# Kernel tuning notes

Hardware: AMD Instinct MI355X
Metric: run time of the kernel (lower is better)

The kernel has to match this reference:

```python
import math
import jax, jax.numpy as jnp
import numpy as np

B, S, HID = 2, 1024, 4096
NH, NKV, HD = 32, 8, 128
G = NH // NKV            # query heads per KV head (GQA group size)
PAST = 1024              # tokens already in the cache per sequence
L = PAST + S             # total KV tokens attended per sequence
SLOTS = 16384            # paged KV-cache slots (flat token addressing)
MAXPOS = 8192
THETA = 10000.0


def _rope_table():
    inv_freq = 1.0 / (THETA ** (np.arange(0, HD, 2, dtype=np.float64) / HD))
    freqs = np.arange(MAXPOS, dtype=np.float64)[:, None] * inv_freq[None, :]
    emb = np.concatenate([freqs, freqs], axis=-1)          # [MAXPOS, HD]
    return jnp.asarray(np.stack([np.cos(emb), np.sin(emb)], axis=1), jnp.float32)  # [MAXPOS,2,HD]


def setup_inputs() -> dict:
    key = jax.random.key(0)
    ks = jax.random.split(key, 6)
    hidden_states = jax.random.normal(ks[0], (B, S, HID), jnp.float32)
    kv_cache = jax.random.normal(ks[1], (SLOTS, 2, NKV, HD), jnp.float32)  # [slot, k/v, kv_head, hd]
    rope_cache = _rope_table()
    Wq = jax.random.normal(ks[2], (HID, NH * HD), jnp.float32) * 0.02
    Wk = jax.random.normal(ks[3], (HID, NKV * HD), jnp.float32) * 0.02
    Wv = jax.random.normal(ks[4], (HID, NKV * HD), jnp.float32) * 0.02
    Wo = jax.random.normal(ks[5], (NH * HD, HID), jnp.float32) * 0.02
    position_offsets = jnp.full((B,), PAST, jnp.int32)
    base = jnp.arange(B, dtype=jnp.int32)[:, None] * L            # each seq owns L contiguous slots
    kv_drain_addr_lut = base + PAST + jnp.arange(S, dtype=jnp.int32)[None, :]  # [B,S] write addrs
    kv_lut = base + jnp.arange(L, dtype=jnp.int32)[None, :]                    # [B,L] read addrs
    return {
        "hidden_states": hidden_states, "kv_cache": kv_cache, "rope_cache": rope_cache,
        "Wq": Wq, "Wk": Wk, "Wv": Wv, "Wo": Wo,
        "position_offsets": position_offsets,
        "kv_drain_addr_lut": kv_drain_addr_lut, "kv_lut": kv_lut,
    }


def _apply_rope(x, cos, sin):
    # x: [B, H, S, HD]; cos/sin: [B, 1, S, HD]
    x1, x2 = x[..., : HD // 2], x[..., HD // 2:]
    return x * cos + jnp.concatenate([-x2, x1], axis=-1) * sin


def reference(hidden_states, kv_cache, rope_cache, Wq, Wk, Wv, Wo,
              position_offsets, kv_drain_addr_lut, kv_lut):
    # QKV projections
    q = (hidden_states @ Wq).reshape(B, S, NH, HD).transpose(0, 2, 1, 3)    # [B,NH,S,HD]
    k = (hidden_states @ Wk).reshape(B, S, NKV, HD).transpose(0, 2, 1, 3)   # [B,NKV,S,HD]
    v = (hidden_states @ Wv).reshape(B, S, NKV, HD).transpose(0, 2, 1, 3)
    # RoPE at absolute positions
    pos = position_offsets[:, None] + jnp.arange(S, dtype=jnp.int32)        # [B,S]
    cos = rope_cache[pos, 0][:, None]                                       # [B,1,S,HD]
    sin = rope_cache[pos, 1][:, None]
    q = _apply_rope(q, cos, sin)
    k = _apply_rope(k, cos, sin)
    # LUT-addressed KV-cache drain (copy_kv_block)
    k_tok = k.transpose(0, 2, 1, 3).reshape(B * S, NKV, HD)
    v_tok = v.transpose(0, 2, 1, 3).reshape(B * S, NKV, HD)
    lut = kv_drain_addr_lut.reshape(-1)
    kv_cache = kv_cache.at[lut, 0].set(k_tok).at[lut, 1].set(v_tok)
    # Gather per-sequence KV pages and run grouped (GQA) causal attention
    kv = kv_cache[kv_lut]                                                   # [B,L,2,NKV,HD]
    keys = kv[:, :, 0].transpose(0, 2, 1, 3)                                # [B,NKV,L,HD]
    vals = kv[:, :, 1].transpose(0, 2, 1, 3)
    qg = q.reshape(B, NKV, G, S, HD)
    scores = jnp.einsum('bhgsd,bhld->bhgsl', qg, keys) * (HD ** -0.5)       # [B,NKV,G,S,L]
    kpos = jnp.arange(L, dtype=jnp.int32)
    causal = kpos[None, None, :] <= pos[:, :, None]                         # [B,S,L]
    scores = jnp.where(causal[:, None, None], scores, jnp.float32(-1e30))
    p = jax.nn.softmax(scores, axis=-1)
    out = jnp.einsum('bhgsl,bhld->bhgsd', p, vals).reshape(B, NH, S, HD)
    out = out.transpose(0, 2, 1, 3).reshape(B, S, HID)
    return out @ Wo
```

## Files before the change

kernel.cpp:

```cpp
#include <hip/hip_runtime.h>
#include <hip/hip_bf16.h>
#include <cstdint>
#include <cstddef>

#define B_    2
#define S_    1024
#define HID_  4096
#define NH_   32
#define NKV_  8
#define HD_   128
#define G_    4
#define PAST_ 1024
#define L_    2048
#define NQKV_ 6144

typedef __bf16 bf16_t;
typedef bf16_t bf16x4 __attribute__((ext_vector_type(4)));
typedef bf16_t bf16x8 __attribute__((ext_vector_type(8)));
typedef float  f32x4  __attribute__((ext_vector_type(4)));

__device__ __forceinline__ void gload_lds16(const bf16_t* g, bf16_t* l) {
  __builtin_amdgcn_global_load_lds(
      (const __attribute__((address_space(1))) void*)g,
      (__attribute__((address_space(3))) void*)l, 16, 0, 0);
}

__global__ __launch_bounds__(256) void cvt_bf16x8(const float* __restrict__ src,
                                                  bf16_t* __restrict__ dst) {
  size_t i = ((size_t)blockIdx.x * 256 + threadIdx.x) * 8;
  f32x4 a = *(const f32x4*)(src + i);
  f32x4 b = *(const f32x4*)(src + i + 4);
  bf16x8 o;
#pragma unroll
  for (int j = 0; j < 4; ++j) o[j] = (bf16_t)a[j];
#pragma unroll
  for (int j = 0; j < 4; ++j) o[4 + j] = (bf16_t)b[j];
  *(bf16x8*)(dst + i) = o;
}

__global__ __launch_bounds__(256) void transpose_cvt(const float* __restrict__ src,
                                                     bf16_t* __restrict__ dst,
                                                     int R, int C) {
  __shared__ float T[64][65];
  const int tid = threadIdx.x;
  const int c0 = blockIdx.x * 64;
  const int r0 = blockIdx.y * 64;
#pragma unroll
  for (int i = 0; i < 16; ++i) {
    int idx = i * 256 + tid;
    int lr = idx >> 6, lc = idx & 63;
    T[lr][lc] = src[(size_t)(r0 + lr) * C + c0 + lc];
  }
  __syncthreads();
#pragma unroll
  for (int i = 0; i < 16; ++i) {
    int idx = i * 256 + tid;
    int lr = idx >> 6, lc = idx & 63;
    dst[(size_t)(c0 + lr) * R + r0 + lc] = (bf16_t)T[lc][lr];
  }
}

template <bool OUT_BF16>
__global__ __launch_bounds__(256) void gemm_bt(const bf16_t* __restrict__ A,
                                               const bf16_t* __restrict__ Bt,
                                               void* __restrict__ C, int N, int K) {
  __shared__ bf16_t As[128 * 32];
  __shared__ bf16_t Bs[128 * 32];
  const int tid = threadIdx.x;
  const int lane = tid & 63;
  const int w = tid >> 6;
  const int wm = w >> 1, wn = w & 1;
  const int m0 = blockIdx.y * 128;
  const int n0 = blockIdx.x * 128;
  const int g = lane >> 4;
  const int r16 = lane & 15;

  f32x4 acc[4][4] = {};

  for (int kt = 0; kt < K; kt += 32) {
    __syncthreads();
#pragma unroll
    for (int j = 0; j < 2; ++j) {
      int cbase = (w * 2 + j) * 64;
      int chunk = cbase + lane;
      gload_lds16(A + (size_t)(m0 + (chunk >> 2)) * K + kt + (chunk & 3) * 8,
                  As + cbase * 8);
      gload_lds16(Bt + (size_t)(n0 + (chunk >> 2)) * K + kt + (chunk & 3) * 8,
                  Bs + cbase * 8);
    }
    __syncthreads();
    bf16x8 af[4], bf[4];
#pragma unroll
    for (int i = 0; i < 4; ++i)
      af[i] = *(const bf16x8*)&As[(wm * 64 + i * 16 + r16) * 32 + g * 8];
#pragma unroll
    for (int i = 0; i < 4; ++i)
      bf[i] = *(const bf16x8*)&Bs[(wn * 64 + i * 16 + r16) * 32 + g * 8];
#pragma unroll
    for (int i = 0; i < 4; ++i)
#pragma unroll
      for (int j2 = 0; j2 < 4; ++j2)
        acc[i][j2] = __builtin_amdgcn_mfma_f32_16x16x32_bf16(af[i], bf[j2],
                                                             acc[i][j2], 0, 0, 0);
  }

#pragma unroll
  for (int i = 0; i < 4; ++i)
#pragma unroll
    for (int j2 = 0; j2 < 4; ++j2)
#pragma unroll
      for (int r = 0; r < 4; ++r) {
        int row = m0 + wm * 64 + i * 16 + g * 4 + r;
        int col = n0 + wn * 64 + j2 * 16 + r16;
        if (OUT_BF16)
          ((bf16_t*)C)[(size_t)row * N + col] = (bf16_t)acc[i][j2][r];
        else
          ((float*)C)[(size_t)row * N + col] = acc[i][j2][r];
      }
}

__global__ __launch_bounds__(256) void rope_pack(const bf16_t* __restrict__ QKV,
                                                 const float* __restrict__ rope,
                                                 bf16_t* __restrict__ Qb,
                                                 bf16_t* __restrict__ Kb) {
  const int tok = blockIdx.x;
  const int head = blockIdx.y * 2 + (threadIdx.x >> 7);
  const int d = threadIdx.x & 127;
  const int b = tok >> 10, s = tok & 1023;
  const int pos = PAST_ + s;
  const int off = head < NH_ ? head * HD_ : HID_ + (head - NH_) * HD_;
  const bf16_t* row = QKV + (size_t)tok * NQKV_;
  float x = (float)row[off + d];
  int dp = d < 64 ? d + 64 : d - 64;
  float xp = (float)row[off + dp];
  float c = rope[(size_t)(pos * 2) * HD_ + d];
  float sn = rope[(size_t)(pos * 2 + 1) * HD_ + d];
  float out = d < 64 ? x * c - xp * sn : x * c + xp * sn;
  if (head < NH_)
    Qb[((size_t)(b * NH_ + head) * S_ + s) * HD_ + d] = (bf16_t)out;
  else
    Kb[((size_t)(b * NKV_ + (head - NH_)) * L_ + PAST_ + s) * HD_ + d] = (bf16_t)out;
}

__global__ __launch_bounds__(256) void past_kv(const float* __restrict__ cache,
                                               const int* __restrict__ kv_lut,
                                               bf16_t* __restrict__ Kb,
                                               bf16_t* __restrict__ Vt) {
  __shared__ bf16_t Vs[128][72];
  const int tid = threadIdx.x;
  const int lt = blockIdx.x & 15;
  const int h = (blockIdx.x >> 4) & 7;
  const int b = blockIdx.x >> 7;
  const int l0 = lt * 64;
#pragma unroll
  for (int i = 0; i < 32; ++i) {
    int idx = i * 256 + tid;
    int l = idx >> 7, d = idx & 127;
    int slot = kv_lut[b * L_ + l0 + l];
    float kv = cache[((size_t)slot * 2 * NKV_ + h) * HD_ + d];
    float vv = cache[(((size_t)slot * 2 + 1) * NKV_ + h) * HD_ + d];
    Kb[((size_t)(b * NKV_ + h) * L_ + l0 + l) * HD_ + d] = (bf16_t)kv;
    Vs[d][l] = (bf16_t)vv;
  }
  __syncthreads();
#pragma unroll
  for (int i = 0; i < 32; ++i) {
    int idx = i * 256 + tid;
    int d = idx >> 6, l = idx & 63;
    Vt[((size_t)(b * NKV_ + h) * HD_ + d) * L_ + l0 + l] = Vs[d][l];
  }
}

__global__ __launch_bounds__(256) void v_pack(const bf16_t* __restrict__ QKV,
                                              bf16_t* __restrict__ Vt) {
  __shared__ bf16_t Vs[128][72];
  const int tid = threadIdx.x;
  const int st = blockIdx.x & 15;
  const int h = (blockIdx.x >> 4) & 7;
  const int b = blockIdx.x >> 7;
  const int s0 = st * 64;
#pragma unroll
  for (int i = 0; i < 32; ++i) {
    int idx = i * 256 + tid;
    int sl = idx >> 7, d = idx & 127;
    Vs[d][sl] = QKV[(size_t)(b * S_ + s0 + sl) * NQKV_ + HID_ + NKV_ * HD_ + h * HD_ + d];
  }
  __syncthreads();
#pragma unroll
  for (int i = 0; i < 32; ++i) {
    int idx = i * 256 + tid;
    int d = idx >> 6, l = idx & 63;
    Vt[((size_t)(b * NKV_ + h) * HD_ + d) * L_ + PAST_ + s0 + l] = Vs[d][l];
  }
}

__global__ __launch_bounds__(512) void attn(const bf16_t* __restrict__ Qb,
                                            const bf16_t* __restrict__ Kb,
                                            const bf16_t* __restrict__ Vt,
                                            bf16_t* __restrict__ Ctx) {
  __shared__ bf16_t smem[40960];

  const int tid = threadIdx.x;
  const int lane = tid & 63;
  const int w = tid >> 6;
  const int g = lane >> 4;
  const int r16 = lane & 15;
  const int rx = r16 & 7;

  const int id = blockIdx.x;
  const int kh = id & 7;
  const int b = (id >> 3) & 1;
  const int qh = (id >> 4) & 3;
  const int grp = id >> 6;
  const int qc = grp < 4 ? 7 - grp : grp - 4;
  const int h = kh * G_ + qh;

  const int s0w = qc * 128 + w * 16;

  const bf16_t* qp = Qb + ((size_t)(b * NH_ + h) * S_ + s0w + r16) * HD_ + g * 8;
  bf16x8 qf[4];
#pragma unroll
  for (int ks = 0; ks < 4; ++ks) qf[ks] = *(const bf16x8*)(qp + ks * 32);

  const bf16_t* kbase = Kb + (size_t)(b * NKV_ + kh) * L_ * HD_;
  const bf16_t* vbase = Vt + (size_t)(b * NKV_ + kh) * HD_ * L_;

  const int slot0 = w * 2;
  const int kl0 = slot0 * 4 + (lane >> 4);
  const int kc0 = (lane & 15) ^ (kl0 & 7);
  const int kl1 = kl0 + 4;
  const int kc1 = (lane & 15) ^ (kl1 & 7);
  const int vd0 = slot0 * 8 + (lane >> 3);
  const int vc0 = (lane & 7) ^ (vd0 & 7);
  const int vd1 = vd0 + 8;
  const int vc1 = (lane & 7) ^ (vd1 & 7);

  float m_run = -1e30f;
  float s_run = 0.f;
  f32x4 acc_o[8] = {};

  const float scale = 0.08838834764831845f;
  const int qpos_base = PAST_ + s0w;
  const int qpos = qpos_base + r16;
  const int nt_ = 18 + 2 * qc;

  {
    bf16_t* Kd = smem;
    bf16_t* Vd = smem + 16384;
    gload_lds16(kbase + (size_t)kl0 * HD_ + kc0 * 8, Kd + slot0 * 512);
    gload_lds16(kbase + (size_t)kl1 * HD_ + kc1 * 8, Kd + (slot0 + 1) * 512);
    gload_lds16(vbase + (size_t)vd0 * L_ + vc0 * 8, Vd + slot0 * 512);
    gload_lds16(vbase + (size_t)vd1 * L_ + vc1 * 8, Vd + (slot0 + 1) * 512);
  }
  __syncthreads();

  for (int t = 0; t < nt_; ++t) {
    const int cur = t & 1;
    const int lt = t * 64;

    if (t + 1 < nt_) {
      const int ltn = lt + 64;
      bf16_t* Kd = smem + (cur ^ 1) * 8192;
      bf16_t* Vd = smem + 16384 + (cur ^ 1) * 8192;
      gload_lds16(kbase + (size_t)(ltn + kl0) * HD_ + kc0 * 8, Kd + slot0 * 512);
      gload_lds16(kbase + (size_t)(ltn + kl1) * HD_ + kc1 * 8, Kd + (slot0 + 1) * 512);
      gload_lds16(vbase + (size_t)vd0 * L_ + ltn + vc0 * 8, Vd + slot0 * 512);
      gload_lds16(vbase + (size_t)vd1 * L_ + ltn + vc1 * 8, Vd + (slot0 + 1) * 512);
    }

    const bf16_t* Kc = smem + cur * 8192;
    const bf16_t* Vc = smem + 16384 + cur * 8192;
    bf16_t* Pw = smem + 32768 + w * 1024;

    f32x4 sc[4] = {};
#pragma unroll
    for (int nt = 0; nt < 4; ++nt) {
#pragma unroll
      for (int ks = 0; ks < 4; ++ks) {
        bf16x8 kf = *(const bf16x8*)&Kc[(nt * 16 + r16) * 128 + (((ks * 4 + g) ^ rx) << 3)];
        sc[nt] = __builtin_amdgcn_mfma_f32_16x16x32_bf16(kf, qf[ks], sc[nt], 0, 0, 0);
      }
    }

    const bool need_mask = (lt + 63) > qpos_base;
    float sv[4][4];
    float tmax = -1e30f;
#pragma unroll
    for (int nt = 0; nt < 4; ++nt)
#pragma unroll
      for (int r = 0; r < 4; ++r) {
        float v = sc[nt][r] * scale;
        if (need_mask) {
          int l = lt + nt * 16 + g * 4 + r;
          if (l > qpos) v = -1e30f;
        }
        sv[nt][r] = v;
        tmax = fmaxf(tmax, v);
      }
    tmax = fmaxf(tmax, __shfl_xor(tmax, 16, 64));
    tmax = fmaxf(tmax, __shfl_xor(tmax, 32, 64));

    if (!__all(tmax <= m_run + 8.f)) {
      float newm = fmaxf(m_run, tmax);
      float alpha = __expf(m_run - newm);
      m_run = newm;
      s_run *= alpha;
#pragma unroll
      for (int r = 0; r < 4; ++r) {
        float a = __shfl(alpha, g * 4 + r, 64);
#pragma unroll
        for (int d8 = 0; d8 < 8; ++d8) acc_o[d8][r] *= a;
      }
    }

    float psum = 0.f;
#pragma unroll
    for (int nt = 0; nt < 4; ++nt) {
      bf16x4 pk;
#pragma unroll
      for (int r = 0; r < 4; ++r) {
        float pv = __expf(sv[nt][r] - m_run);
        psum += pv;
        pk[r] = (bf16_t)pv;
      }
      *(bf16x4*)&Pw[r16 * 64 + (((nt * 2 + (g >> 1)) ^ rx) << 3) + (g & 1) * 4] = pk;
    }
    psum += __shfl_xor(psum, 16, 64);
    psum += __shfl_xor(psum, 32, 64);
    s_run += psum;

#pragma unroll
    for (int ks2 = 0; ks2 < 2; ++ks2) {
      bf16x8 pa = *(const bf16x8*)&Pw[r16 * 64 + (((ks2 * 4 + g) ^ rx) << 3)];
#pragma unroll
      for (int d8 = 0; d8 < 8; ++d8) {
        bf16x8 vf = *(const bf16x8*)&Vc[(d8 * 16 + r16) * 64 + (((ks2 * 4 + g) ^ rx) << 3)];
        acc_o[d8] = __builtin_amdgcn_mfma_f32_16x16x32_bf16(pa, vf, acc_o[d8], 0, 0, 0);
      }
    }

    __syncthreads();
  }

  float inv[4];
#pragma unroll
  for (int r = 0; r < 4; ++r) inv[r] = 1.f / __shfl(s_run, g * 4 + r, 64);
#pragma unroll
  for (int d8 = 0; d8 < 8; ++d8)
#pragma unroll
    for (int r = 0; r < 4; ++r) {
      int tok = b * S_ + s0w + g * 4 + r;
      int col = h * HD_ + d8 * 16 + r16;
      Ctx[(size_t)tok * HID_ + col] = (bf16_t)(acc_o[d8][r] * inv[r]);
    }
}

extern "C" void kernel_launch(void* const* d_in, const int* in_sizes, int n_in,
                              void* d_out, int out_size, void* d_ws, size_t ws_size,
                              hipStream_t stream) {
  const float* hidden = (const float*)d_in[0];
  const float* kv_cache = (const float*)d_in[1];
  const float* rope = (const float*)d_in[2];
  const float* Wq = (const float*)d_in[3];
  const float* Wk = (const float*)d_in[4];
  const float* Wv = (const float*)d_in[5];
  const float* Wo = (const float*)d_in[6];
  const int* kv_lut = (const int*)d_in[9];
  float* out = (float*)d_out;

  bf16_t* Xb = (bf16_t*)d_ws;
  bf16_t* Wcat = Xb + (size_t)2048 * 4096;
  bf16_t* Wot = Wcat + (size_t)6144 * 4096;
  bf16_t* QKVb = Wot + (size_t)4096 * 4096;
  bf16_t* Qb = QKVb + (size_t)2048 * 6144;
  bf16_t* Kb = Qb + (size_t)B_ * NH_ * S_ * HD_;
  bf16_t* Vt = Kb + (size_t)B_ * NKV_ * L_ * HD_;
  bf16_t* Ctx = Xb;

  cvt_bf16x8<<<4096, 256, 0, stream>>>(hidden, Xb);
  transpose_cvt<<<dim3(64, 64), 256, 0, stream>>>(Wq, Wcat, 4096, 4096);
  transpose_cvt<<<dim3(16, 64), 256, 0, stream>>>(Wk, Wcat + (size_t)4096 * 4096, 4096, 1024);
  transpose_cvt<<<dim3(16, 64), 256, 0, stream>>>(Wv, Wcat + (size_t)5120 * 4096, 4096, 1024);
  transpose_cvt<<<dim3(64, 64), 256, 0, stream>>>(Wo, Wot, 4096, 4096);

  gemm_bt<true><<<dim3(48, 16), 256, 0, stream>>>(Xb, Wcat, QKVb, NQKV_, HID_);

  rope_pack<<<dim3(2048, 20), 256, 0, stream>>>(QKVb, rope, Qb, Kb);
  past_kv<<<256, 256, 0, stream>>>(kv_cache, kv_lut, Kb, Vt);
  v_pack<<<256, 256, 0, stream>>>(QKVb, Vt);

  attn<<<512, 512, 0, stream>>>(Qb, Kb, Vt, Ctx);

  gemm_bt<false><<<dim3(32, 16), 256, 0, stream>>>(Ctx, Wot, out, HID_, HID_);
}
```

Before: 417.6 us.

## Replace GEMM with 256-row double-buffered swizzled LDS kernel and XCD-aware tiling

Replaces the 128x128 single-buffered GEMM with a 512-thread kernel using 256xBN tiles (BN=192 for QKV, 128 for output projection). It double-buffers K=64 stages in LDS with XOR-swizzled layout, uses explicit vmcnt waits plus raw barriers, and raises MFMA priority. Blocks are remapped so neighbouring tiles land on the same XCD. The aim is to hide global-to-LDS latency, cut bank conflicts and improve L2 reuse, at the cost of more LDS and registers per block and fragile hand-tuned wait counts.

```diff
diff --git a/kernel.cpp b/kernel.cpp
--- a/kernel.cpp
+++ b/kernel.cpp
@@ -60,62 +60,124 @@
   }
 }
 
-template <bool OUT_BF16>
-__global__ __launch_bounds__(256) void gemm_bt(const bf16_t* __restrict__ A,
-                                               const bf16_t* __restrict__ Bt,
-                                               void* __restrict__ C, int N, int K) {
-  __shared__ bf16_t As[128 * 32];
-  __shared__ bf16_t Bs[128 * 32];
+template <int BN, bool OUT_BF16>
+__global__ __launch_bounds__(512) void gemm8(const bf16_t* __restrict__ A,
+                                             const bf16_t* __restrict__ Bt,
+                                             void* __restrict__ C, int N, int K) {
+  constexpr int BSLAB = BN * 32;
+  constexpr int BUFE = 16384 + 2 * BSLAB;
+  constexpr int NF = BN / 64;
+  constexpr int WN = BN / 4;
+  constexpr int BCH = BN * 4;
+  __shared__ bf16_t sm[2 * BUFE];
+
   const int tid = threadIdx.x;
   const int lane = tid & 63;
   const int w = tid >> 6;
-  const int wm = w >> 1, wn = w & 1;
-  const int m0 = blockIdx.y * 128;
-  const int n0 = blockIdx.x * 128;
+  const int wm = w >> 2, wn = w & 3;
   const int g = lane >> 4;
   const int r16 = lane & 15;
 
-  f32x4 acc[4][4] = {};
-
-  for (int kt = 0; kt < K; kt += 32) {
-    __syncthreads();
+  const int flat = blockIdx.y * 32 + blockIdx.x;
+  const int xcd = flat & 7;
+  const int i2 = flat >> 3;
+  const int tx = xcd * 4 + (i2 & 3);
+  const int ty = i2 >> 2;
+  const int m0 = ty * 256;
+  const int n0 = tx * BN;
+
+  const int NT = K >> 6;
+
+  f32x4 acc[8][NF] = {};
+
+  auto stageA = [&](int T, int j) {
+    bf16_t* base = sm + (T & 1) * BUFE + j * 8192;
+#pragma unroll
+    for (int cj = 0; cj < 2; ++cj) {
+      int c = (w * 2 + cj) * 64 + lane;
+      int p = c * 16;
+      int l = p ^ (((p >> 9) & 1) << 5);
+      int row = l >> 6, colb = l & 63;
+      gload_lds16(A + (size_t)(m0 + row) * K + T * 64 + j * 32 + (colb >> 1),
+                  base + (w * 2 + cj) * 512);
+    }
+  };
+  auto stageB = [&](int T, int j) {
+    bf16_t* base = sm + (T & 1) * BUFE + 16384 + j * BSLAB;
+#pragma unroll
+    for (int cj = 0; cj < (BCH + 511) / 512; ++cj) {
+      int cbase = cj * 512 + w * 64;
+      if (cbase < BCH) {
+        int c = cbase + lane;
+        int p = c * 16;
+        int l = p ^ (((p >> 9) & 1) << 5);
+        int row = l >> 6, colb = l & 63;
+        gload_lds16(Bt + (size_t)(n0 + row) * K + T * 64 + j * 32 + (colb >> 1),
+                    base + cbase * 8);
+      }
+    }
+  };
+  auto waitbar = [&]() {
+    if (BN == 192) {
+      if (w < 4) asm volatile("s_waitcnt vmcnt(4)" ::: "memory");
+      else       asm volatile("s_waitcnt vmcnt(3)" ::: "memory");
+    } else {
+      asm volatile("s_waitcnt vmcnt(3)" ::: "memory");
+    }
+    asm volatile("s_barrier" ::: "memory");
+  };
+
+  stageA(0, 0); stageB(0, 0);
+  stageA(0, 1); stageB(0, 1);
+  waitbar();
+
+#pragma unroll 2
+  for (int T = 0; T < NT; ++T) {
+    const bf16_t* abuf = sm + (T & 1) * BUFE;
+    const bf16_t* bbuf = abuf + 16384;
 #pragma unroll
     for (int j = 0; j < 2; ++j) {
-      int cbase = (w * 2 + j) * 64;
-      int chunk = cbase + lane;
-      gload_lds16(A + (size_t)(m0 + (chunk >> 2)) * K + kt + (chunk & 3) * 8,
-                  As + cbase * 8);
-      gload_lds16(Bt + (size_t)(n0 + (chunk >> 2)) * K + kt + (chunk & 3) * 8,
-                  Bs + cbase * 8);
-    }
-    __syncthreads();
-    bf16x8 af[4], bf[4];
-#pragma unroll
-    for (int i = 0; i < 4; ++i)
-      af[i] = *(const bf16x8*)&As[(wm * 64 + i * 16 + r16) * 32 + g * 8];
-#pragma unroll
-    for (int i = 0; i < 4; ++i)
-      bf[i] = *(const bf16x8*)&Bs[(wn * 64 + i * 16 + r16) * 32 + g * 8];
-#pragma unroll
-    for (int i = 0; i < 4; ++i)
-#pragma unroll
-      for (int j2 = 0; j2 < 4; ++j2)
-        acc[i][j2] = __builtin_amdgcn_mfma_f32_16x16x32_bf16(af[i], bf[j2],
-                                                             acc[i][j2], 0, 0, 0);
-  }
-
-#pragma unroll
-  for (int i = 0; i < 4; ++i)
-#pragma unroll
-    for (int j2 = 0; j2 < 4; ++j2)
+      const bf16_t* as = abuf + j * 8192;
+      const bf16_t* bs = bbuf + j * BSLAB;
+      bf16x8 af[8];
+      bf16x8 bfr[NF];
+#pragma unroll
+      for (int m = 0; m < 8; ++m) {
+        int a = (wm * 128 + m * 16 + r16) * 64 + g * 16;
+        a ^= ((a >> 9) & 1) << 5;
+        af[m] = *(const bf16x8*)((const char*)as + a);
+      }
+#pragma unroll
+      for (int n = 0; n < NF; ++n) {
+        int a = (wn * WN + n * 16 + r16) * 64 + g * 16;
+        a ^= ((a >> 9) & 1) << 5;
+        bfr[n] = *(const bf16x8*)((const char*)bs + a);
+      }
+      if (T + 1 < NT) { stageA(T + 1, j); stageB(T + 1, j); }
+      __builtin_amdgcn_s_setprio(1);
+#pragma unroll
+      for (int m = 0; m < 8; ++m)
+#pragma unroll
+        for (int n = 0; n < NF; ++n)
+          acc[m][n] = __builtin_amdgcn_mfma_f32_16x16x32_bf16(af[m], bfr[n],
+                                                              acc[m][n], 0, 0, 0);
+      __builtin_amdgcn_s_setprio(0);
+      waitbar();
+    }
+  }
+
+#pragma unroll
+  for (int m = 0; m < 8; ++m)
+#pragma unroll
+    for (int n = 0; n < NF; ++n)
 #pragma unroll
       for (int r = 0; r < 4; ++r) {
-        int row = m0 + wm * 64 + i * 16 + g * 4 + r;
-        int col = n0 + wn * 64 + j2 * 16 + r16;
+        int row = m0 + wm * 128 + m * 16 + g * 4 + r;
+        int col = n0 + wn * WN + n * 16 + r16;
         if (OUT_BF16)
-          ((bf16_t*)C)[(size_t)row * N + col] = (bf16_t)acc[i][j2][r];
+          ((bf16_t*)C)[(size_t)row * N + col] = (bf16_t)acc[m][n][r];
         else
-          ((float*)C)[(size_t)row * N + col] = acc[i][j2][r];
+          ((float*)C)[(size_t)row * N + col] = acc[m][n][r];
       }
 }
 
@@ -383,7 +445,7 @@
   transpose_cvt<<<dim3(16, 64), 256, 0, stream>>>(Wv, Wcat + (size_t)5120 * 4096, 4096, 1024);
   transpose_cvt<<<dim3(64, 64), 256, 0, stream>>>(Wo, Wot, 4096, 4096);
 
-  gemm_bt<true><<<dim3(48, 16), 256, 0, stream>>>(Xb, Wcat, QKVb, NQKV_, HID_);
+  gemm8<192, true><<<dim3(32, 8), 512, 0, stream>>>(Xb, Wcat, QKVb, NQKV_, HID_);
 
   rope_pack<<<dim3(2048, 20), 256, 0, stream>>>(QKVb, rope, Qb, Kb);
   past_kv<<<256, 256, 0, stream>>>(kv_cache, kv_lut, Kb, Vt);
@@ -391,5 +453,5 @@
 
   attn<<<512, 512, 0, stream>>>(Qb, Kb, Vt, Ctx);
 
-  gemm_bt<false><<<dim3(32, 16), 256, 0, stream>>>(Ctx, Wot, out, HID_, HID_);
-}
+  gemm8<128, false><<<dim3(32, 8), 512, 0, stream>>>(Ctx, Wot, out, HID_, HID_);
+}
```

Result: faster. 351.5 us (-15.8%).
